# Kernel optimization log

Hardware: AMD Instinct MI355X
Metric: run time of the kernel (lower is better)

Reference implementation:

```python
import jax, jax.numpy as jnp
import numpy as np

N = 50000
E = 625000
D = 128
L = 3
BN_EPS = 1e-5


def setup_inputs() -> dict:
    key = jax.random.key(0)
    ks = jax.random.split(key, 12)
    x = jax.random.normal(ks[0], (N, D), dtype=jnp.float32)
    edge_index = jax.random.randint(ks[1], (2, E), 0, N, dtype=jnp.int64)
    s = 1.0 / np.sqrt(D)
    W1 = jax.random.uniform(ks[2], (L, D, D), jnp.float32, -s, s)
    b1 = jax.random.uniform(ks[3], (L, D), jnp.float32, -s, s)
    W2 = jax.random.uniform(ks[4], (L, D, D), jnp.float32, -s, s)
    b2 = jax.random.uniform(ks[5], (L, D), jnp.float32, -s, s)
    eps = jnp.zeros((L,), jnp.float32)  # GINConv train_eps init 0
    gamma = jnp.ones((L, D), jnp.float32)
    beta = jnp.zeros((L, D), jnp.float32)
    Wl = jax.random.uniform(ks[6], (L, D, D), jnp.float32, -s, s)
    bl = jax.random.uniform(ks[7], (L, D), jnp.float32, -s, s)
    return {"x": x, "edge_index": edge_index, "W1": W1, "b1": b1, "W2": W2,
            "b2": b2, "eps": eps, "gamma": gamma, "beta": beta, "Wl": Wl, "bl": bl}


def reference(x, edge_index, W1, b1, W2, b2, eps, gamma, beta, Wl, bl):
    src, dst = edge_index[0], edge_index[1]
    xs = [x]
    h = x
    for i in range(L):
        # GIN aggregation: sum of neighbor (source) features at target nodes
        agg = jax.ops.segment_sum(h[src], dst, num_segments=N)  # [N, D]
        z = (1.0 + eps[i]) * h + agg
        # MLP: Linear -> ReLU -> Linear
        z = jax.nn.relu(z @ W1[i] + b1[i]) @ W2[i] + b2[i]
        # BatchNorm1d (training mode: batch stats, biased variance)
        mu = jnp.mean(z, axis=0)
        var = jnp.mean((z - mu) ** 2, axis=0)
        z = gamma[i] * (z - mu) * jax.lax.rsqrt(var + BN_EPS) + beta[i]
        if i != 0:
            z = z + xs[-1]
        h = jax.nn.relu(z)
        xs.append(h)
    outs = [xs[i + 1] @ Wl[i] + bl[i] for i in range(L)]
    return jnp.concatenate(outs, axis=-1)  # [N, L*D]
```

## Files before the change

kernel.cpp:

```cpp
#include <hip/hip_runtime.h>
#include <hip/hip_bf16.h>
#include <stdint.h>

#define NN 50000
#define NE 625000
#define DD 128
#define NL 3
#define GB 391

typedef __bf16 bf16x8 __attribute__((ext_vector_type(8)));
typedef float f32x4 __attribute__((ext_vector_type(4)));

__device__ __forceinline__ float bflo(uint32_t u) { return __uint_as_float(u << 16); }
__device__ __forceinline__ float bfhi(uint32_t u) { return __uint_as_float(u & 0xffff0000u); }
__device__ __forceinline__ uint16_t f2bf(float f) {
    __hip_bfloat16 h = __float2bfloat16(f);
    return __builtin_bit_cast(uint16_t, h);
}
__device__ __forceinline__ uint32_t pack2(float lo, float hi) {
    return (uint32_t)f2bf(lo) | ((uint32_t)f2bf(hi) << 16);
}

__global__ void k_hist(const int* __restrict__ dstv, int* __restrict__ deg) {
    int e = blockIdx.x * 256 + threadIdx.x;
    if (e < NE) atomicAdd(&deg[dstv[e]], 1);
}

__global__ __launch_bounds__(512) void k_bsum(const int* __restrict__ deg, int* __restrict__ bsum) {
    __shared__ int s[512];
    int i = blockIdx.x * 512 + threadIdx.x;
    int v = (i < NN) ? deg[i] : 0;
    s[threadIdx.x] = v;
    __syncthreads();
    for (int st = 256; st > 0; st >>= 1) {
        if (threadIdx.x < st) s[threadIdx.x] += s[threadIdx.x + st];
        __syncthreads();
    }
    if (threadIdx.x == 0) bsum[blockIdx.x] = s[0];
}

__global__ __launch_bounds__(128) void k_scanbs(const int* __restrict__ bsum, int* __restrict__ bsoff) {
    __shared__ int s[128];
    int t = threadIdx.x;
    int v = (t < 98) ? bsum[t] : 0;
    s[t] = v;
    __syncthreads();
    for (int st = 1; st < 128; st <<= 1) {
        int a = (t >= st) ? s[t - st] : 0;
        __syncthreads();
        s[t] += a;
        __syncthreads();
    }
    if (t < 98) bsoff[t] = s[t] - v;
}

__global__ __launch_bounds__(512) void k_scan2(int* __restrict__ deg_cursor,
                                               const int* __restrict__ bsoff,
                                               int* __restrict__ rowptr) {
    __shared__ int s[512];
    int t = threadIdx.x;
    int i = blockIdx.x * 512 + t;
    int v = (i < NN) ? deg_cursor[i] : 0;
    s[t] = v;
    __syncthreads();
    for (int st = 1; st < 512; st <<= 1) {
        int a = (t >= st) ? s[t - st] : 0;
        __syncthreads();
        s[t] += a;
        __syncthreads();
    }
    if (i < NN) {
        int excl = bsoff[blockIdx.x] + s[t] - v;
        rowptr[i] = excl;
        deg_cursor[i] = excl;
        if (i == NN - 1) rowptr[NN] = excl + v;
    }
}

__global__ void k_fill(const int* __restrict__ srcv, const int* __restrict__ dstv,
                       int* __restrict__ cursor, int* __restrict__ colv) {
    int e = blockIdx.x * 256 + threadIdx.x;
    if (e < NE) {
        int d = dstv[e];
        int p = atomicAdd(&cursor[d], 1);
        colv[p] = srcv[e];
    }
}

#define WCONV_BLOCKS 576
__global__ void k_prep(const float* __restrict__ x, uint16_t* __restrict__ hb,
                       int* __restrict__ cursor,
                       const float* __restrict__ W1, const float* __restrict__ W2,
                       const float* __restrict__ Wl, uint16_t* __restrict__ Wb) {
    int b = blockIdx.x;
    if (b < WCONV_BLOCKS) {
        int id = b * 256 + threadIdx.x;
        int m = id >> 14;
        int r = id & 16383;
        int k = r >> 7;
        int col = r & 127;
        const float* src;
        if (m < 3) src = W1 + m * 16384;
        else if (m < 6) src = W2 + (m - 3) * 16384;
        else src = Wl + (m - 6) * 16384;
        float v = src[k * 128 + col];
        Wb[m * 16384 + col * 128 + (k ^ ((col & 7) << 3))] = f2bf(v);
        return;
    }
    int id = (b - WCONV_BLOCKS) * 256 + threadIdx.x;
    if (id < NN) cursor[id] = 0;
    int base = id * 4;
    if (base >= NN * DD) return;
    float4 v = *(const float4*)(x + base);
    uint2 st;
    st.x = pack2(v.x, v.y);
    st.y = pack2(v.z, v.w);
    *(uint2*)(hb + base) = st;
}

__global__ __launch_bounds__(256) void k_agg(const uint16_t* __restrict__ hb,
                                             const int* __restrict__ rowptr,
                                             const int* __restrict__ colv,
                                             const float* __restrict__ epsp, int layer,
                                             uint16_t* __restrict__ zb,
                                             float* __restrict__ bnsum) {
    if (blockIdx.x == 0) bnsum[threadIdx.x] = 0.f;
    int g = (blockIdx.x * 256 + threadIdx.x) >> 4;
    int l16 = threadIdx.x & 15;
    if (g >= NN) return;
    float onepe = 1.0f + epsp[layer];
    int beg = rowptr[g], end = rowptr[g + 1];
    const uint4* hp = (const uint4*)hb;
    float a0 = 0.f, a1 = 0.f, a2 = 0.f, a3 = 0.f, a4 = 0.f, a5 = 0.f, a6 = 0.f, a7 = 0.f;
    int j = beg;
    for (; j + 3 < end; j += 4) {
        int s0 = colv[j];
        int s1 = colv[j + 1];
        int s2 = colv[j + 2];
        int s3 = colv[j + 3];
        uint4 u0 = hp[(size_t)s0 * 16 + l16];
        uint4 u1 = hp[(size_t)s1 * 16 + l16];
        uint4 u2 = hp[(size_t)s2 * 16 + l16];
        uint4 u3 = hp[(size_t)s3 * 16 + l16];
        a0 += bflo(u0.x); a1 += bfhi(u0.x); a2 += bflo(u0.y); a3 += bfhi(u0.y);
        a4 += bflo(u0.z); a5 += bfhi(u0.z); a6 += bflo(u0.w); a7 += bfhi(u0.w);
        a0 += bflo(u1.x); a1 += bfhi(u1.x); a2 += bflo(u1.y); a3 += bfhi(u1.y);
        a4 += bflo(u1.z); a5 += bfhi(u1.z); a6 += bflo(u1.w); a7 += bfhi(u1.w);
        a0 += bflo(u2.x); a1 += bfhi(u2.x); a2 += bflo(u2.y); a3 += bfhi(u2.y);
        a4 += bflo(u2.z); a5 += bfhi(u2.z); a6 += bflo(u2.w); a7 += bfhi(u2.w);
        a0 += bflo(u3.x); a1 += bfhi(u3.x); a2 += bflo(u3.y); a3 += bfhi(u3.y);
        a4 += bflo(u3.z); a5 += bfhi(u3.z); a6 += bflo(u3.w); a7 += bfhi(u3.w);
    }
    for (; j < end; ++j) {
        int s0 = colv[j];
        uint4 u = hp[(size_t)s0 * 16 + l16];
        a0 += bflo(u.x); a1 += bfhi(u.x); a2 += bflo(u.y); a3 += bfhi(u.y);
        a4 += bflo(u.z); a5 += bfhi(u.z); a6 += bflo(u.w); a7 += bfhi(u.w);
    }
    uint4 hu = hp[(size_t)g * 16 + l16];
    a0 = fmaf(onepe, bflo(hu.x), a0); a1 = fmaf(onepe, bfhi(hu.x), a1);
    a2 = fmaf(onepe, bflo(hu.y), a2); a3 = fmaf(onepe, bfhi(hu.y), a3);
    a4 = fmaf(onepe, bflo(hu.z), a4); a5 = fmaf(onepe, bfhi(hu.z), a5);
    a6 = fmaf(onepe, bflo(hu.w), a6); a7 = fmaf(onepe, bfhi(hu.w), a7);
    uint4 st;
    st.x = pack2(a0, a1); st.y = pack2(a2, a3);
    st.z = pack2(a4, a5); st.w = pack2(a6, a7);
    ((uint4*)zb)[(size_t)g * 16 + l16] = st;
}

__global__ __launch_bounds__(256) void k_mlp(const uint16_t* __restrict__ A,
                                             const uint16_t* __restrict__ W1img,
                                             const uint16_t* __restrict__ W2img,
                                             const float* __restrict__ b1,
                                             const float* __restrict__ b2,
                                             float* __restrict__ bnsum,
                                             uint16_t* __restrict__ z2b) {
    __shared__ uint16_t ldsW[16384];
    __shared__ uint16_t ldsT[16384];
    int tid = threadIdx.x;
    int wid = tid >> 6, lane = tid & 63;

    bf16x8 w2r[8];
#pragma unroll
    for (int it = 0; it < 8; ++it) w2r[it] = *(const bf16x8*)(W2img + (it * 256 + tid) * 8);

#pragma unroll
    for (int it = 0; it < 8; ++it) {
        int idx = (it * 256 + tid) * 8;
        *(bf16x8*)(&ldsW[idx]) = *(const bf16x8*)(W1img + idx);
    }
    __syncthreads();

    const int brow = blockIdx.x * 128;
    const int m0 = wid * 32;
    const int l15 = lane & 15;
    const int lhi = lane >> 4;

    f32x4 acc[2][8];
    f32x4 zero = {0.f, 0.f, 0.f, 0.f};
#pragma unroll
    for (int m = 0; m < 2; ++m)
#pragma unroll
        for (int n = 0; n < 8; ++n) acc[m][n] = zero;

    const char* Ab = (const char*)A;
#pragma unroll
    for (int kk = 0; kk < 4; ++kk) {
        int kbyte = kk * 64 + (lhi << 4);
        bf16x8 afrag[2];
#pragma unroll
        for (int m = 0; m < 2; ++m) {
            int row = brow + m0 + m * 16 + l15;
            if (row >= NN) row = NN - 1;
            afrag[m] = *(const bf16x8*)(Ab + (size_t)row * 256 + kbyte);
        }
#pragma unroll
        for (int n = 0; n < 8; ++n) {
            int col = n * 16 + l15;
            int addr = col * 256 + (kbyte ^ ((col & 7) << 4));
            bf16x8 bfrag = *(const bf16x8*)((const char*)ldsW + addr);
            acc[0][n] = __builtin_amdgcn_mfma_f32_16x16x32_bf16(afrag[0], bfrag, acc[0][n], 0, 0, 0);
            acc[1][n] = __builtin_amdgcn_mfma_f32_16x16x32_bf16(afrag[1], bfrag, acc[1][n], 0, 0, 0);
        }
    }

    {
        float bc[8];
#pragma unroll
        for (int n = 0; n < 8; ++n) bc[n] = b1[n * 16 + l15];
#pragma unroll
        for (int m = 0; m < 2; ++m) {
            int rbase = m0 + m * 16 + (lhi << 2);
#pragma unroll
            for (int r = 0; r < 4; ++r) {
                int row = rbase + r;
#pragma unroll
                for (int n = 0; n < 8; ++n) {
                    float v = fmaxf(acc[m][n][r] + bc[n], 0.f);
                    int col = n * 16 + l15;
                    int byteoff = row * 256 + ((col * 2) ^ ((row & 7) << 4));
                    *(uint16_t*)((char*)ldsT + byteoff) = f2bf(v);
                }
            }
        }
    }
    __syncthreads();

#pragma unroll
    for (int it = 0; it < 8; ++it) *(bf16x8*)(&ldsW[(it * 256 + tid) * 8]) = w2r[it];
    __syncthreads();

#pragma unroll
    for (int m = 0; m < 2; ++m)
#pragma unroll
        for (int n = 0; n < 8; ++n) acc[m][n] = zero;

#pragma unroll
    for (int kk = 0; kk < 4; ++kk) {
        int kbyte = kk * 64 + (lhi << 4);
        bf16x8 afrag[2];
#pragma unroll
        for (int m = 0; m < 2; ++m) {
            int rowl = m0 + m * 16 + l15;
            afrag[m] = *(const bf16x8*)((const char*)ldsT + rowl * 256 + (kbyte ^ ((rowl & 7) << 4)));
        }
#pragma unroll
        for (int n = 0; n < 8; ++n) {
            int col = n * 16 + l15;
            int addr = col * 256 + (kbyte ^ ((col & 7) << 4));
            bf16x8 bfrag = *(const bf16x8*)((const char*)ldsW + addr);
            acc[0][n] = __builtin_amdgcn_mfma_f32_16x16x32_bf16(afrag[0], bfrag, acc[0][n], 0, 0, 0);
            acc[1][n] = __builtin_amdgcn_mfma_f32_16x16x32_bf16(afrag[1], bfrag, acc[1][n], 0, 0, 0);
        }
    }

    float bc2[8];
#pragma unroll
    for (int n = 0; n < 8; ++n) bc2[n] = b2[n * 16 + l15];

    float s1[8], s2[8];
#pragma unroll
    for (int n = 0; n < 8; ++n) { s1[n] = 0.f; s2[n] = 0.f; }

#pragma unroll
    for (int m = 0; m < 2; ++m) {
        int rbase = brow + m0 + m * 16 + (lhi << 2);
#pragma unroll
        for (int r = 0; r < 4; ++r) {
            int row = rbase + r;
            bool ok = row < NN;
#pragma unroll
            for (int n = 0; n < 8; ++n) {
                float v = acc[m][n][r] + bc2[n];
                if (ok) {
                    z2b[(size_t)row * 128 + n * 16 + l15] = f2bf(v);
                    s1[n] += v;
                    s2[n] += v * v;
                }
            }
        }
    }

    __syncthreads();
    float* ls = (float*)ldsT;
    ls[tid] = 0.f;
    __syncthreads();
#pragma unroll
    for (int n = 0; n < 8; ++n) {
        float a1 = s1[n] + __shfl_xor(s1[n], 16);
        a1 += __shfl_xor(a1, 32);
        float a2 = s2[n] + __shfl_xor(s2[n], 16);
        a2 += __shfl_xor(a2, 32);
        if (lane < 16) {
            atomicAdd(&ls[n * 16 + lane], a1);
            atomicAdd(&ls[128 + n * 16 + lane], a2);
        }
    }
    __syncthreads();
    atomicAdd(&bnsum[tid], ls[tid]);
}

__global__ __launch_bounds__(256) void k_apply(const uint16_t* __restrict__ z2b,
                                               const uint16_t* __restrict__ hin,
                                               const float* __restrict__ bnsum,
                                               const float* __restrict__ gamma,
                                               const float* __restrict__ beta, int layer,
                                               uint16_t* __restrict__ hout) {
    __shared__ float sA[128], sB[128];
    int tid = threadIdx.x;
    if (tid < 128) {
        float mu = bnsum[tid] * (1.0f / NN);
        float var = bnsum[128 + tid] * (1.0f / NN) - mu * mu;
        float a = gamma[layer * 128 + tid] * rsqrtf(var + 1e-5f);
        sA[tid] = a;
        sB[tid] = beta[layer * 128 + tid] - mu * a;
    }
    __syncthreads();
    int id = blockIdx.x * 256 + tid;
    int base = id * 4;
    if (base >= NN * DD) return;
    int c = base & 127;
    uint2 zu = *(const uint2*)(z2b + base);
    float4 av = *(const float4*)(sA + c);
    float4 bv = *(const float4*)(sB + c);
    float v0 = fmaf(av.x, bflo(zu.x), bv.x);
    float v1 = fmaf(av.y, bfhi(zu.x), bv.y);
    float v2 = fmaf(av.z, bflo(zu.y), bv.z);
    float v3 = fmaf(av.w, bfhi(zu.y), bv.w);
    if (layer > 0) {
        uint2 h = *(const uint2*)(hin + base);
        v0 += bflo(h.x);
        v1 += bfhi(h.x);
        v2 += bflo(h.y);
        v3 += bfhi(h.y);
    }
    v0 = fmaxf(v0, 0.f);
    v1 = fmaxf(v1, 0.f);
    v2 = fmaxf(v2, 0.f);
    v3 = fmaxf(v3, 0.f);
    uint2 st;
    st.x = pack2(v0, v1);
    st.y = pack2(v2, v3);
    *(uint2*)(hout + base) = st;
}

__global__ __launch_bounds__(256) void k_outgemm(const uint16_t* __restrict__ h1,
                                                 const uint16_t* __restrict__ h2,
                                                 const uint16_t* __restrict__ h3,
                                                 const uint16_t* __restrict__ Wb6,
                                                 const float* __restrict__ bl,
                                                 float* __restrict__ out) {
    __shared__ uint16_t lds[16384];
    int layer = blockIdx.x / GB;
    int blk = blockIdx.x - layer * GB;
    const uint16_t* A = (layer == 0) ? h1 : ((layer == 1) ? h2 : h3);
    const uint16_t* Wimg = Wb6 + layer * 16384;
    const float* bias = bl + layer * 128;

    int tid = threadIdx.x;
    int wid = tid >> 6, lane = tid & 63;
#pragma unroll
    for (int it = 0; it < 8; ++it) {
        int idx = (it * 256 + tid) * 8;
        bf16x8 v = *(const bf16x8*)(Wimg + idx);
        *(bf16x8*)(&lds[idx]) = v;
    }
    __syncthreads();

    const int brow = blk * 128;
    const int m0 = wid * 32;
    const int l15 = lane & 15;
    const int lhi = lane >> 4;

    f32x4 acc[2][8];
    f32x4 zero = {0.f, 0.f, 0.f, 0.f};
#pragma unroll
    for (int m = 0; m < 2; ++m)
#pragma unroll
        for (int n = 0; n < 8; ++n) acc[m][n] = zero;

    const char* Ab = (const char*)A;
#pragma unroll
    for (int kk = 0; kk < 4; ++kk) {
        int kbyte = kk * 64 + (lhi << 4);
        bf16x8 afrag[2];
#pragma unroll
        for (int m = 0; m < 2; ++m) {
            int row = brow + m0 + m * 16 + l15;
            if (row >= NN) row = NN - 1;
            afrag[m] = *(const bf16x8*)(Ab + (size_t)row * 256 + kbyte);
        }
#pragma unroll
        for (int n = 0; n < 8; ++n) {
            int col = n * 16 + l15;
            int addr = col * 256 + (kbyte ^ ((col & 7) << 4));
            bf16x8 bfrag = *(const bf16x8*)((const char*)lds + addr);
            acc[0][n] = __builtin_amdgcn_mfma_f32_16x16x32_bf16(afrag[0], bfrag, acc[0][n], 0, 0, 0);
            acc[1][n] = __builtin_amdgcn_mfma_f32_16x16x32_bf16(afrag[1], bfrag, acc[1][n], 0, 0, 0);
        }
    }

    float bcol[8];
#pragma unroll
    for (int n = 0; n < 8; ++n) bcol[n] = bias[n * 16 + l15];

#pragma unroll
    for (int m = 0; m < 2; ++m) {
        int rbase = brow + m0 + m * 16 + (lhi << 2);
#pragma unroll
        for (int r = 0; r < 4; ++r) {
            int row = rbase + r;
            if (row < NN) {
#pragma unroll
                for (int n = 0; n < 8; ++n) {
                    float v = acc[m][n][r] + bcol[n];
                    out[(size_t)row * (NL * DD) + layer * 128 + n * 16 + l15] = v;
                }
            }
        }
    }
}

extern "C" void kernel_launch(void* const* d_in, const int* in_sizes, int n_in,
                              void* d_out, int out_size, void* d_ws, size_t ws_size,
                              hipStream_t stream) {
    const float* x = (const float*)d_in[0];
    const int* ei = (const int*)d_in[1];
    const float* W1 = (const float*)d_in[2];
    const float* b1 = (const float*)d_in[3];
    const float* W2 = (const float*)d_in[4];
    const float* b2 = (const float*)d_in[5];
    const float* epsp = (const float*)d_in[6];
    const float* gamma = (const float*)d_in[7];
    const float* beta = (const float*)d_in[8];
    const float* Wl = (const float*)d_in[9];
    const float* bl = (const float*)d_in[10];
    float* out = (float*)d_out;

    char* w = (char*)d_ws;
    size_t off = 0;
    auto take = [&](size_t b) -> char* {
        char* p = w + off;
        off += (b + 255) & ~(size_t)255;
        return p;
    };
    uint16_t* hb[4];
    for (int i = 0; i < 4; ++i) hb[i] = (uint16_t*)take((size_t)NN * DD * 2);
    uint16_t* zb = (uint16_t*)take((size_t)NN * DD * 2);
    uint16_t* z2b = (uint16_t*)take((size_t)NN * DD * 2);
    int* rowptr = (int*)take((size_t)(NN + 1) * 4);
    int* cursor = (int*)take((size_t)NN * 4);
    int* colv = (int*)take((size_t)NE * 4);
    int* bsum = (int*)take(128 * 4);
    int* bsoff = (int*)take(128 * 4);
    uint16_t* Wb = (uint16_t*)take(9 * 16384 * 2);
    float* bnsum = (float*)take(256 * 4);

    const int* srcv = ei;
    const int* dstv = ei + NE;

    const int x2bf_blocks = (NN * DD / 4 + 255) / 256;
    k_prep<<<WCONV_BLOCKS + x2bf_blocks, 256, 0, stream>>>(x, hb[0], cursor, W1, W2, Wl, Wb);

    k_hist<<<(NE + 255) / 256, 256, 0, stream>>>(dstv, cursor);
    k_bsum<<<98, 512, 0, stream>>>(cursor, bsum);
    k_scanbs<<<1, 128, 0, stream>>>(bsum, bsoff);
    k_scan2<<<98, 512, 0, stream>>>(cursor, bsoff, rowptr);
    k_fill<<<(NE + 255) / 256, 256, 0, stream>>>(srcv, dstv, cursor, colv);

    const int agg_blocks = (NN * 16 + 255) / 256;

    for (int l = 0; l < NL; ++l) {
        k_agg<<<agg_blocks, 256, 0, stream>>>(hb[l], rowptr, colv, epsp, l, zb, bnsum);
        k_mlp<<<GB, 256, 0, stream>>>(zb, Wb + l * 16384, Wb + (3 + l) * 16384,
                                      b1 + l * 128, b2 + l * 128, bnsum, z2b);
        k_apply<<<x2bf_blocks, 256, 0, stream>>>(z2b, hb[l], bnsum, gamma, beta,
                                                 l, hb[l + 1]);
    }
    k_outgemm<<<NL * GB, 256, 0, stream>>>(hb[1], hb[2], hb[3], Wb + 6 * 16384, bl, out);
}
```

Baseline: 263.3 us.

## Replace three-kernel CSR scan with single atomic-offset scan and unroll aggregation by eight

The separate block-sum, block-offset scan and final scan kernels are merged into one kernel. Each block scans its degrees locally and claims a global base offset with an atomicAdd, and a per-row end array replaces rowptr[g+1]. Segments are no longer ordered by node, but the aggregation only needs each row's begin and end. This removes two kernel launches and their dependencies from the preprocessing chain. The aggregation loop also gains an 8-way unrolled gather so more independent loads are in flight, which may raise register use.

```diff
diff --git a/kernel.cpp b/kernel.cpp
--- a/kernel.cpp
+++ b/kernel.cpp
@@ -26,41 +26,15 @@
     if (e < NE) atomicAdd(&deg[dstv[e]], 1);
 }
 
-__global__ __launch_bounds__(512) void k_bsum(const int* __restrict__ deg, int* __restrict__ bsum) {
+__global__ __launch_bounds__(512) void k_scan1(int* __restrict__ cursor ,
+                                               int* __restrict__ rowptr,
+                                               int* __restrict__ rowend,
+                                               int* __restrict__ gcount) {
     __shared__ int s[512];
-    int i = blockIdx.x * 512 + threadIdx.x;
-    int v = (i < NN) ? deg[i] : 0;
-    s[threadIdx.x] = v;
-    __syncthreads();
-    for (int st = 256; st > 0; st >>= 1) {
-        if (threadIdx.x < st) s[threadIdx.x] += s[threadIdx.x + st];
-        __syncthreads();
-    }
-    if (threadIdx.x == 0) bsum[blockIdx.x] = s[0];
-}
-
-__global__ __launch_bounds__(128) void k_scanbs(const int* __restrict__ bsum, int* __restrict__ bsoff) {
-    __shared__ int s[128];
-    int t = threadIdx.x;
-    int v = (t < 98) ? bsum[t] : 0;
-    s[t] = v;
-    __syncthreads();
-    for (int st = 1; st < 128; st <<= 1) {
-        int a = (t >= st) ? s[t - st] : 0;
-        __syncthreads();
-        s[t] += a;
-        __syncthreads();
-    }
-    if (t < 98) bsoff[t] = s[t] - v;
-}
-
-__global__ __launch_bounds__(512) void k_scan2(int* __restrict__ deg_cursor,
-                                               const int* __restrict__ bsoff,
-                                               int* __restrict__ rowptr) {
-    __shared__ int s[512];
+    __shared__ int base;
     int t = threadIdx.x;
     int i = blockIdx.x * 512 + t;
-    int v = (i < NN) ? deg_cursor[i] : 0;
+    int v = (i < NN) ? cursor[i] : 0;
     s[t] = v;
     __syncthreads();
     for (int st = 1; st < 512; st <<= 1) {
@@ -69,11 +43,13 @@
         s[t] += a;
         __syncthreads();
     }
+    if (t == 511) base = atomicAdd(gcount, s[511]);
+    __syncthreads();
     if (i < NN) {
-        int excl = bsoff[blockIdx.x] + s[t] - v;
-        rowptr[i] = excl;
-        deg_cursor[i] = excl;
-        if (i == NN - 1) rowptr[NN] = excl + v;
+        int b = base + s[t] - v;
+        rowptr[i] = b;
+        rowend[i] = b + v;
+        cursor[i] = b;
     }
 }
 
@@ -89,7 +65,7 @@
 
 #define WCONV_BLOCKS 576
 __global__ void k_prep(const float* __restrict__ x, uint16_t* __restrict__ hb,
-                       int* __restrict__ cursor,
+                       int* __restrict__ cursor, int* __restrict__ gcount,
                        const float* __restrict__ W1, const float* __restrict__ W2,
                        const float* __restrict__ Wl, uint16_t* __restrict__ Wb) {
     int b = blockIdx.x;
@@ -108,6 +84,7 @@
         return;
     }
     int id = (b - WCONV_BLOCKS) * 256 + threadIdx.x;
+    if (id == 0) *gcount = 0;
     if (id < NN) cursor[id] = 0;
     int base = id * 4;
     if (base >= NN * DD) return;
@@ -118,8 +95,13 @@
     *(uint2*)(hb + base) = st;
 }
 
+#define ACC8(u) \
+    a0 += bflo(u.x); a1 += bfhi(u.x); a2 += bflo(u.y); a3 += bfhi(u.y); \
+    a4 += bflo(u.z); a5 += bfhi(u.z); a6 += bflo(u.w); a7 += bfhi(u.w);
+
 __global__ __launch_bounds__(256) void k_agg(const uint16_t* __restrict__ hb,
                                              const int* __restrict__ rowptr,
+                                             const int* __restrict__ rowend,
                                              const int* __restrict__ colv,
                                              const float* __restrict__ epsp, int layer,
                                              uint16_t* __restrict__ zb,
@@ -129,10 +111,30 @@
     int l16 = threadIdx.x & 15;
     if (g >= NN) return;
     float onepe = 1.0f + epsp[layer];
-    int beg = rowptr[g], end = rowptr[g + 1];
+    int beg = rowptr[g], end = rowend[g];
     const uint4* hp = (const uint4*)hb;
     float a0 = 0.f, a1 = 0.f, a2 = 0.f, a3 = 0.f, a4 = 0.f, a5 = 0.f, a6 = 0.f, a7 = 0.f;
     int j = beg;
+    for (; j + 7 < end; j += 8) {
+        int s0 = colv[j];
+        int s1 = colv[j + 1];
+        int s2 = colv[j + 2];
+        int s3 = colv[j + 3];
+        int s4 = colv[j + 4];
+        int s5 = colv[j + 5];
+        int s6 = colv[j + 6];
+        int s7 = colv[j + 7];
+        uint4 u0 = hp[(size_t)s0 * 16 + l16];
+        uint4 u1 = hp[(size_t)s1 * 16 + l16];
+        uint4 u2 = hp[(size_t)s2 * 16 + l16];
+        uint4 u3 = hp[(size_t)s3 * 16 + l16];
+        uint4 u4 = hp[(size_t)s4 * 16 + l16];
+        uint4 u5 = hp[(size_t)s5 * 16 + l16];
+        uint4 u6 = hp[(size_t)s6 * 16 + l16];
+        uint4 u7 = hp[(size_t)s7 * 16 + l16];
+        ACC8(u0) ACC8(u1) ACC8(u2) ACC8(u3)
+        ACC8(u4) ACC8(u5) ACC8(u6) ACC8(u7)
+    }
     for (; j + 3 < end; j += 4) {
         int s0 = colv[j];
         int s1 = colv[j + 1];
@@ -142,20 +144,12 @@
         uint4 u1 = hp[(size_t)s1 * 16 + l16];
         uint4 u2 = hp[(size_t)s2 * 16 + l16];
         uint4 u3 = hp[(size_t)s3 * 16 + l16];
-        a0 += bflo(u0.x); a1 += bfhi(u0.x); a2 += bflo(u0.y); a3 += bfhi(u0.y);
-        a4 += bflo(u0.z); a5 += bfhi(u0.z); a6 += bflo(u0.w); a7 += bfhi(u0.w);
-        a0 += bflo(u1.x); a1 += bfhi(u1.x); a2 += bflo(u1.y); a3 += bfhi(u1.y);
-        a4 += bflo(u1.z); a5 += bfhi(u1.z); a6 += bflo(u1.w); a7 += bfhi(u1.w);
-        a0 += bflo(u2.x); a1 += bfhi(u2.x); a2 += bflo(u2.y); a3 += bfhi(u2.y);
-        a4 += bflo(u2.z); a5 += bfhi(u2.z); a6 += bflo(u2.w); a7 += bfhi(u2.w);
-        a0 += bflo(u3.x); a1 += bfhi(u3.x); a2 += bflo(u3.y); a3 += bfhi(u3.y);
-        a4 += bflo(u3.z); a5 += bfhi(u3.z); a6 += bflo(u3.w); a7 += bfhi(u3.w);
+        ACC8(u0) ACC8(u1) ACC8(u2) ACC8(u3)
     }
     for (; j < end; ++j) {
         int s0 = colv[j];
         uint4 u = hp[(size_t)s0 * 16 + l16];
-        a0 += bflo(u.x); a1 += bfhi(u.x); a2 += bflo(u.y); a3 += bfhi(u.y);
-        a4 += bflo(u.z); a5 += bfhi(u.z); a6 += bflo(u.w); a7 += bfhi(u.w);
+        ACC8(u)
     }
     uint4 hu = hp[(size_t)g * 16 + l16];
     a0 = fmaf(onepe, bflo(hu.x), a0); a1 = fmaf(onepe, bfhi(hu.x), a1);
@@ -468,30 +462,29 @@
     for (int i = 0; i < 4; ++i) hb[i] = (uint16_t*)take((size_t)NN * DD * 2);
     uint16_t* zb = (uint16_t*)take((size_t)NN * DD * 2);
     uint16_t* z2b = (uint16_t*)take((size_t)NN * DD * 2);
-    int* rowptr = (int*)take((size_t)(NN + 1) * 4);
+    int* rowptr = (int*)take((size_t)NN * 4);
+    int* rowend = (int*)take((size_t)NN * 4);
     int* cursor = (int*)take((size_t)NN * 4);
     int* colv = (int*)take((size_t)NE * 4);
-    int* bsum = (int*)take(128 * 4);
-    int* bsoff = (int*)take(128 * 4);
     uint16_t* Wb = (uint16_t*)take(9 * 16384 * 2);
     float* bnsum = (float*)take(256 * 4);
+    int* gcount = (int*)take(256);
 
     const int* srcv = ei;
     const int* dstv = ei + NE;
 
     const int x2bf_blocks = (NN * DD / 4 + 255) / 256;
-    k_prep<<<WCONV_BLOCKS + x2bf_blocks, 256, 0, stream>>>(x, hb[0], cursor, W1, W2, Wl, Wb);
+    k_prep<<<WCONV_BLOCKS + x2bf_blocks, 256, 0, stream>>>(x, hb[0], cursor, gcount,
+                                                           W1, W2, Wl, Wb);
 
     k_hist<<<(NE + 255) / 256, 256, 0, stream>>>(dstv, cursor);
-    k_bsum<<<98, 512, 0, stream>>>(cursor, bsum);
-    k_scanbs<<<1, 128, 0, stream>>>(bsum, bsoff);
-    k_scan2<<<98, 512, 0, stream>>>(cursor, bsoff, rowptr);
+    k_scan1<<<98, 512, 0, stream>>>(cursor, rowptr, rowend, gcount);
     k_fill<<<(NE + 255) / 256, 256, 0, stream>>>(srcv, dstv, cursor, colv);
 
     const int agg_blocks = (NN * 16 + 255) / 256;
 
     for (int l = 0; l < NL; ++l) {
-        k_agg<<<agg_blocks, 256, 0, stream>>>(hb[l], rowptr, colv, epsp, l, zb, bnsum);
+        k_agg<<<agg_blocks, 256, 0, stream>>>(hb[l], rowptr, rowend, colv, epsp, l, zb, bnsum);
         k_mlp<<<GB, 256, 0, stream>>>(zb, Wb + l * 16384, Wb + (3 + l) * 16384,
                                       b1 + l * 128, b2 + l * 128, bnsum, z2b);
         k_apply<<<x2bf_blocks, 256, 0, stream>>>(z2b, hb[l], bnsum, gamma, beta,
```

New measurement: 266.2 us. Within noise of the previous version (+1.1%).
